# Kernel tuning notes

Hardware: AMD Instinct MI355X
Metric: run time of the kernel (lower is better)

Reference implementation:

```python
import jax, jax.numpy as jnp
import numpy as np

N = [100000, 50000, 25000, 12500]   # node frontier per hop (src of layer l = N[l], dst = N[l+1])
E = [800000, 400000, 200000]        # edges per sampled bipartite subgraph
IN, HID = 256, 256
N_LAYERS = 3


def setup_inputs() -> dict:
    key = jax.random.key(0)
    ks = jax.random.split(key, 20)
    inp = {"x": jax.random.normal(ks[0], (N[0], IN), dtype=jnp.float32)}
    for l in range(N_LAYERS):
        src = jax.random.randint(ks[1 + 2 * l], (E[l],), 0, N[l])
        dst = jax.random.randint(ks[2 + 2 * l], (E[l],), 0, N[l + 1])
        inp[f"edge_index_{l}"] = jnp.stack([src, dst]).astype(jnp.int64)
    for l in range(N_LAYERS):
        din = IN if l == 0 else HID
        s = din ** -0.5
        inp[f"W_l_{l}"] = jax.random.normal(ks[7 + 3 * l], (din, HID), jnp.float32) * s
        inp[f"b_l_{l}"] = jnp.zeros((HID,), jnp.float32)
        inp[f"W_r_{l}"] = jax.random.normal(ks[8 + 3 * l], (din, HID), jnp.float32) * s
    return inp


def _sage_layer(h, edge_index, num_dst, W_l, b_l, W_r):
    # PyG SAGEConv with mean aggregation:
    #   out = lin_l(mean_{j in N(i)} h_j) + lin_r(h_i),  h_i = h[:num_dst]
    src, dst = edge_index[0], edge_index[1]
    msg = h[src]                                                    # [E, d] gather
    summed = jax.ops.segment_sum(msg, dst, num_segments=num_dst)    # [num_dst, d]
    cnt = jax.ops.segment_sum(jnp.ones_like(dst, jnp.float32), dst, num_segments=num_dst)
    mean = summed / jnp.maximum(cnt, 1.0)[:, None]
    return mean @ W_l + b_l + h[:num_dst] @ W_r


def reference(x, edge_index_0, edge_index_1, edge_index_2,
              W_l_0, b_l_0, W_r_0, W_l_1, b_l_1, W_r_1, W_l_2, b_l_2, W_r_2):
    edges = [edge_index_0, edge_index_1, edge_index_2]
    params = [(W_l_0, b_l_0, W_r_0), (W_l_1, b_l_1, W_r_1), (W_l_2, b_l_2, W_r_2)]
    h = x
    for l in range(N_LAYERS):
        Wl, bl, Wr = params[l]
        h = _sage_layer(h, edges[l], N[l + 1], Wl, bl, Wr)
        if l != N_LAYERS - 1:
            h = jax.nn.relu(h)
    return h
```

## Files before the change

kernel.cpp:

```cpp
#include <hip/hip_runtime.h>
#include <hip/hip_bf16.h>

typedef __attribute__((ext_vector_type(8))) short bf16x8;
typedef __attribute__((ext_vector_type(4))) float f32x4;

__device__ inline unsigned short f2bf(float f) {
    union { float f; unsigned u; } v; v.f = f;
    unsigned r = v.u + 0x7fff + ((v.u >> 16) & 1);
    return (unsigned short)(r >> 16);
}
__device__ inline float bf2f(unsigned short u) {
    union { unsigned u; float f; } v; v.u = (unsigned)u << 16;
    return v.f;
}

#define SEG0_OFF 0
#define SEG1_OFF 50176
#define SEG2_OFF 75264
#define SEG_TOT  87808
#define NB0 196
#define NB1 98
#define NB2 49
#define NB_TOT 343
#define E_TOT 1400000

__constant__ const int c_segoff[3] = {SEG0_OFF, SEG1_OFF, SEG2_OFF};
__constant__ const int c_segM[3]   = {50000, 25000, 12500};
__constant__ const int c_Es[3]     = {800000, 400000, 200000};
__constant__ const int c_eoff[3]   = {0, 800000, 1200000};

__global__ void cvt_kernel(const float* __restrict__ x, unsigned short* __restrict__ xb, int n4) {
    int i = blockIdx.x * blockDim.x + threadIdx.x;
    if (i >= n4) return;
    float4 v = ((const float4*)x)[i];
    ushort4 o = { f2bf(v.x), f2bf(v.y), f2bf(v.z), f2bf(v.w) };
    ((ushort4*)xb)[i] = o;
}


__global__ void hist_all_kernel(const int* __restrict__ e0, const int* __restrict__ e1,
                                const int* __restrict__ e2, int* __restrict__ cnt) {
    int e = blockIdx.x * blockDim.x + threadIdx.x;
    if (e >= E_TOT) return;
    int l, el; const int* ex;
    if (e < 800000)       { l = 0; el = e;           ex = e0; }
    else if (e < 1200000) { l = 1; el = e - 800000;  ex = e1; }
    else                  { l = 2; el = e - 1200000; ex = e2; }
    int d = ex[c_Es[l] + el];
    atomicAdd(&cnt[c_segoff[l] + d], 1);
}

__device__ inline void seg_of_block(int b, int& seg, int& lb) {
    if (b < NB0)            { seg = 0; lb = b; }
    else if (b < NB0 + NB1) { seg = 1; lb = b - NB0; }
    else                    { seg = 2; lb = b - NB0 - NB1; }
}

__global__ void partial_kernel(const int* __restrict__ cnt, int* __restrict__ bsum) {
    int seg, lb; seg_of_block(blockIdx.x, seg, lb);
    __shared__ int sh[256];
    int t = threadIdx.x;
    sh[t] = cnt[c_segoff[seg] + lb * 256 + t];
    __syncthreads();
    #pragma unroll
    for (int off = 128; off > 0; off >>= 1) {
        if (t < off) sh[t] += sh[t + off];
        __syncthreads();
    }
    if (t == 0) bsum[seg * 256 + lb] = sh[0];
}

__global__ void scanb_kernel(int* __restrict__ bsum, int* __restrict__ rowptr) {
    const int nb[3] = {NB0, NB1, NB2};
    int s = blockIdx.x, t = threadIdx.x;
    __shared__ int sh[256];
    int v = (t < nb[s]) ? bsum[s * 256 + t] : 0;
    sh[t] = v;
    __syncthreads();
    #pragma unroll
    for (int off = 1; off < 256; off <<= 1) {
        int u = (t >= off) ? sh[t - off] : 0;
        __syncthreads();
        sh[t] += u;
        __syncthreads();
    }
    if (t < nb[s]) bsum[s * 256 + t] = sh[t] - v;
    if (t == 0) rowptr[c_segoff[s] + c_segM[s]] = c_Es[s];
}

__global__ void emit_kernel(const int* __restrict__ cnt, const int* __restrict__ bsum,
                            int* __restrict__ rowptr, int* __restrict__ cursor) {
    int seg, lb; seg_of_block(blockIdx.x, seg, lb);
    __shared__ int sh[256];
    int t = threadIdx.x;
    int li = lb * 256 + t;
    int idx = c_segoff[seg] + li;
    int v = cnt[idx];
    sh[t] = v;
    __syncthreads();
    #pragma unroll
    for (int off = 1; off < 256; off <<= 1) {
        int u = (t >= off) ? sh[t - off] : 0;
        __syncthreads();
        sh[t] += u;
        __syncthreads();
    }
    int excl = sh[t] - v + bsum[seg * 256 + lb];
    if (li < c_segM[seg]) { rowptr[idx] = excl; cursor[idx] = excl; }
}

__global__ void fill_all_kernel(const int* __restrict__ e0, const int* __restrict__ e1,
                                const int* __restrict__ e2,
                                int* __restrict__ cursor, int* __restrict__ eids) {
    int e = blockIdx.x * blockDim.x + threadIdx.x;
    if (e >= E_TOT) return;
    int l, el; const int* ex;
    if (e < 800000)       { l = 0; el = e;           ex = e0; }
    else if (e < 1200000) { l = 1; el = e - 800000;  ex = e1; }
    else                  { l = 2; el = e - 1200000; ex = e2; }
    int d = ex[c_Es[l] + el];
    int pos = atomicAdd(&cursor[c_segoff[l] + d], 1);
    eids[c_eoff[l] + pos] = ex[el];
}

__global__ void agg_pack_kernel(const unsigned short* __restrict__ hb,
                                const int* __restrict__ rowptr,
                                const int* __restrict__ eids,
                                int M, int Mpad,
                                unsigned short* __restrict__ X) {
    int lane = threadIdx.x & 63;
    int row = blockIdx.x * (blockDim.x >> 6) + (threadIdx.x >> 6);
    if (row >= Mpad) return;
    ushort4* Xv = (ushort4*)X;
    const ushort4* hv = (const ushort4*)hb;
    if (row >= M) {
        ushort4 z = {0, 0, 0, 0};
        Xv[(size_t)row * 128 + lane] = z;
        Xv[(size_t)row * 128 + 64 + lane] = z;
        return;
    }
    int beg = rowptr[row], end = rowptr[row + 1];
    float a0 = 0, a1 = 0, a2 = 0, a3 = 0;
    float b0 = 0, b1 = 0, b2 = 0, b3 = 0;
    int j = beg;
    for (; j + 4 <= end; j += 4) {
        int i0 = eids[j], i1 = eids[j + 1], i2 = eids[j + 2], i3 = eids[j + 3];
        ushort4 v0 = hv[(size_t)i0 * 64 + lane];
        ushort4 v1 = hv[(size_t)i1 * 64 + lane];
        ushort4 v2 = hv[(size_t)i2 * 64 + lane];
        ushort4 v3 = hv[(size_t)i3 * 64 + lane];
        a0 += bf2f(v0.x) + bf2f(v2.x); a1 += bf2f(v0.y) + bf2f(v2.y);
        a2 += bf2f(v0.z) + bf2f(v2.z); a3 += bf2f(v0.w) + bf2f(v2.w);
        b0 += bf2f(v1.x) + bf2f(v3.x); b1 += bf2f(v1.y) + bf2f(v3.y);
        b2 += bf2f(v1.z) + bf2f(v3.z); b3 += bf2f(v1.w) + bf2f(v3.w);
    }
    for (; j < end; ++j) {
        ushort4 v = hv[(size_t)eids[j] * 64 + lane];
        a0 += bf2f(v.x); a1 += bf2f(v.y); a2 += bf2f(v.z); a3 += bf2f(v.w);
    }
    float inv = 1.0f / fmaxf((float)(end - beg), 1.0f);
    ushort4 m;
    m.x = f2bf((a0 + b0) * inv); m.y = f2bf((a1 + b1) * inv);
    m.z = f2bf((a2 + b2) * inv); m.w = f2bf((a3 + b3) * inv);
    Xv[(size_t)row * 128 + lane] = m;
    Xv[(size_t)row * 128 + 64 + lane] = hv[(size_t)row * 64 + lane];
}

__global__ void convw_kernel(const float* __restrict__ Wl0, const float* __restrict__ Wr0,
                             const float* __restrict__ Wl1, const float* __restrict__ Wr1,
                             const float* __restrict__ Wl2, const float* __restrict__ Wr2,
                             unsigned short* __restrict__ Wsw) {
    int gid = blockIdx.x * blockDim.x + threadIdx.x;
    int l = gid >> 17;
    int r = gid & 131071;
    int k = r >> 8, c = r & 255;
    const float* W;
    if (k < 256) W = (l == 0) ? Wl0 : (l == 1) ? Wl1 : Wl2;
    else         W = (l == 0) ? Wr0 : (l == 1) ? Wr1 : Wr2;
    float v = W[(size_t)(k & 255) * 256 + c];
    Wsw[(size_t)l * 131072 + (size_t)(k >> 3) * 2048 + c * 8 + (k & 7)] = f2bf(v);
}

__global__ void gemm_kernel(const unsigned short* __restrict__ X,
                            const unsigned short* __restrict__ Wsw,
                            const float* __restrict__ bias,
                            float* __restrict__ outf, unsigned short* __restrict__ outb,
                            int M, int relu) {
    int tid = threadIdx.x;
    int wid = tid >> 6, lane = tid & 63;
    int lr = lane & 15, lg = lane >> 4;
    int r0 = blockIdx.x * 64;
    int c0 = wid * 64;
    f32x4 acc[4][4] = {};
    #pragma unroll 2
    for (int k0 = 0; k0 < 512; k0 += 32) {
        bf16x8 a[4];
        #pragma unroll
        for (int mf = 0; mf < 4; ++mf)
            a[mf] = *(const bf16x8*)(X + (size_t)(r0 + mf * 16 + lr) * 512 + k0 + lg * 8);
        #pragma unroll
        for (int nf = 0; nf < 4; ++nf) {
            bf16x8 b = *(const bf16x8*)(Wsw + ((size_t)(k0 >> 3) + lg) * 2048 +
                                        (size_t)(c0 + nf * 16 + lr) * 8);
            #pragma unroll
            for (int mf = 0; mf < 4; ++mf)
                acc[mf][nf] = __builtin_amdgcn_mfma_f32_16x16x32_bf16(a[mf], b, acc[mf][nf], 0, 0, 0);
        }
    }
    #pragma unroll
    for (int nf = 0; nf < 4; ++nf) {
        int col = c0 + nf * 16 + lr;
        float bv = bias[col];
        #pragma unroll
        for (int mf = 0; mf < 4; ++mf) {
            #pragma unroll
            for (int j = 0; j < 4; ++j) {
                int row = r0 + mf * 16 + lg * 4 + j;
                if (row < M) {
                    float v = acc[mf][nf][j] + bv;
                    if (relu) v = fmaxf(v, 0.0f);
                    size_t idx = (size_t)row * 256 + col;
                    if (outf) outf[idx] = v;
                    else      outb[idx] = f2bf(v);
                }
            }
        }
    }
}

extern "C" void kernel_launch(void* const* d_in, const int* in_sizes, int n_in,
                              void* d_out, int out_size, void* d_ws, size_t ws_size,
                              hipStream_t stream) {
    const float* x  = (const float*)d_in[0];
    const int*   e0 = (const int*)d_in[1];
    const int*   e1 = (const int*)d_in[2];
    const int*   e2 = (const int*)d_in[3];
    const float* Wl[3] = {(const float*)d_in[4], (const float*)d_in[7], (const float*)d_in[10]};
    const float* bl[3] = {(const float*)d_in[5], (const float*)d_in[8], (const float*)d_in[11]};
    const float* Wr[3] = {(const float*)d_in[6], (const float*)d_in[9], (const float*)d_in[12]};
    float* out = (float*)d_out;

    char* ws = (char*)d_ws;
    unsigned short* X      = (unsigned short*)(ws + 0);
    unsigned short* xb     = (unsigned short*)(ws + 51249152);
    unsigned short* h1b    = (unsigned short*)(ws + 102449152);
    unsigned short* h2b    = (unsigned short*)(ws + 128049152);
    unsigned short* Wsw    = (unsigned short*)(ws + 140849152);
    int*            cnt    = (int*)(ws + 141635584);
    int*            rowptr = (int*)(ws + 141986816);
    int*            cursor = (int*)(ws + 142338048);
    int*            bsum   = (int*)(ws + 142689280);
    int*            eids   = (int*)(ws + 142693376);

    const int Ns[4] = {100000, 50000, 25000, 12500};
    const int segoff[3] = {SEG0_OFF, SEG1_OFF, SEG2_OFF};
    const int eoff[3] = {0, 800000, 1200000};
    const unsigned short* hsrc[3] = {xb, h1b, h2b};

    hipMemsetAsync(cnt, 0, (size_t)SEG_TOT * 4, stream);
    cvt_kernel<<<(6400000 + 255) / 256, 256, 0, stream>>>(x, xb, 6400000);
    convw_kernel<<<1536, 256, 0, stream>>>(Wl[0], Wr[0], Wl[1], Wr[1], Wl[2], Wr[2], Wsw);

    hist_all_kernel<<<(E_TOT + 255) / 256, 256, 0, stream>>>(e0, e1, e2, cnt);
    partial_kernel<<<NB_TOT, 256, 0, stream>>>(cnt, bsum);
    scanb_kernel<<<3, 256, 0, stream>>>(bsum, rowptr);
    emit_kernel<<<NB_TOT, 256, 0, stream>>>(cnt, bsum, rowptr, cursor);
    fill_all_kernel<<<(E_TOT + 255) / 256, 256, 0, stream>>>(e0, e1, e2, cursor, eids);

    for (int l = 0; l < 3; ++l) {
        int Md = Ns[l + 1];
        int Mpad = (Md + 63) & ~63;
        agg_pack_kernel<<<Mpad / 4, 256, 0, stream>>>(
            hsrc[l], rowptr + segoff[l], eids + eoff[l], Md, Mpad, X);
        float* of = (l == 2) ? out : nullptr;
        unsigned short* ob = (l == 0) ? h1b : (l == 1) ? h2b : nullptr;
        gemm_kernel<<<Mpad / 64, 256, 0, stream>>>(
            X, Wsw + (size_t)l * 131072, bl[l], of, ob, Md, (l < 2) ? 1 : 0);
    }
}
```

Baseline: 586.7 us.

## Fuse prep kernels and record per-edge rank to drop fill atomics

```diff
diff --git a/kernel.cpp b/kernel.cpp
--- a/kernel.cpp
+++ b/kernel.cpp
@@ -23,31 +23,50 @@
 #define NB2 49
 #define NB_TOT 343
 #define E_TOT 1400000
+#define CVT_NB 25000
+#define CONVW_NB 1536
+#define HIST_NB 5469
 
 __constant__ const int c_segoff[3] = {SEG0_OFF, SEG1_OFF, SEG2_OFF};
 __constant__ const int c_segM[3]   = {50000, 25000, 12500};
 __constant__ const int c_Es[3]     = {800000, 400000, 200000};
 __constant__ const int c_eoff[3]   = {0, 800000, 1200000};
 
-__global__ void cvt_kernel(const float* __restrict__ x, unsigned short* __restrict__ xb, int n4) {
-    int i = blockIdx.x * blockDim.x + threadIdx.x;
-    if (i >= n4) return;
-    float4 v = ((const float4*)x)[i];
-    ushort4 o = { f2bf(v.x), f2bf(v.y), f2bf(v.z), f2bf(v.w) };
-    ((ushort4*)xb)[i] = o;
-}
-
-
-__global__ void hist_all_kernel(const int* __restrict__ e0, const int* __restrict__ e1,
-                                const int* __restrict__ e2, int* __restrict__ cnt) {
-    int e = blockIdx.x * blockDim.x + threadIdx.x;
-    if (e >= E_TOT) return;
-    int l, el; const int* ex;
-    if (e < 800000)       { l = 0; el = e;           ex = e0; }
-    else if (e < 1200000) { l = 1; el = e - 800000;  ex = e1; }
-    else                  { l = 2; el = e - 1200000; ex = e2; }
-    int d = ex[c_Es[l] + el];
-    atomicAdd(&cnt[c_segoff[l] + d], 1);
+__global__ void prep_kernel(const float* __restrict__ x, unsigned short* __restrict__ xb,
+                            const float* __restrict__ Wl0, const float* __restrict__ Wr0,
+                            const float* __restrict__ Wl1, const float* __restrict__ Wr1,
+                            const float* __restrict__ Wl2, const float* __restrict__ Wr2,
+                            unsigned short* __restrict__ Wsw,
+                            const int* __restrict__ e0, const int* __restrict__ e1,
+                            const int* __restrict__ e2,
+                            int* __restrict__ cnt, unsigned short* __restrict__ rank) {
+    int b = blockIdx.x, t = threadIdx.x;
+    if (b < CVT_NB) {
+        int i = b * 256 + t;
+        float4 v = ((const float4*)x)[i];
+        ushort4 o = { f2bf(v.x), f2bf(v.y), f2bf(v.z), f2bf(v.w) };
+        ((ushort4*)xb)[i] = o;
+    } else if (b < CVT_NB + CONVW_NB) {
+        int gid = (b - CVT_NB) * 256 + t;
+        int l = gid >> 17;
+        int r = gid & 131071;
+        int k = r >> 8, c = r & 255;
+        const float* W;
+        if (k < 256) W = (l == 0) ? Wl0 : (l == 1) ? Wl1 : Wl2;
+        else         W = (l == 0) ? Wr0 : (l == 1) ? Wr1 : Wr2;
+        float v = W[(size_t)(k & 255) * 256 + c];
+        Wsw[(size_t)l * 131072 + (size_t)(k >> 3) * 2048 + c * 8 + (k & 7)] = f2bf(v);
+    } else {
+        int e = (b - CVT_NB - CONVW_NB) * 256 + t;
+        if (e >= E_TOT) return;
+        int l, el; const int* ex;
+        if (e < 800000)       { l = 0; el = e;           ex = e0; }
+        else if (e < 1200000) { l = 1; el = e - 800000;  ex = e1; }
+        else                  { l = 2; el = e - 1200000; ex = e2; }
+        int d = ex[c_Es[l] + el];
+        int r = atomicAdd(&cnt[c_segoff[l] + d], 1);
+        rank[e] = (unsigned short)r;
+    }
 }
 
 __device__ inline void seg_of_block(int b, int& seg, int& lb) {
@@ -89,7 +108,7 @@
 }
 
 __global__ void emit_kernel(const int* __restrict__ cnt, const int* __restrict__ bsum,
-                            int* __restrict__ rowptr, int* __restrict__ cursor) {
+                            int* __restrict__ rowptr) {
     int seg, lb; seg_of_block(blockIdx.x, seg, lb);
     __shared__ int sh[256];
     int t = threadIdx.x;
@@ -106,12 +125,14 @@
         __syncthreads();
     }
     int excl = sh[t] - v + bsum[seg * 256 + lb];
-    if (li < c_segM[seg]) { rowptr[idx] = excl; cursor[idx] = excl; }
+    if (li < c_segM[seg]) rowptr[idx] = excl;
 }
 
 __global__ void fill_all_kernel(const int* __restrict__ e0, const int* __restrict__ e1,
                                 const int* __restrict__ e2,
-                                int* __restrict__ cursor, int* __restrict__ eids) {
+                                const int* __restrict__ rowptr,
+                                const unsigned short* __restrict__ rank,
+                                int* __restrict__ eids) {
     int e = blockIdx.x * blockDim.x + threadIdx.x;
     if (e >= E_TOT) return;
     int l, el; const int* ex;
@@ -119,7 +140,7 @@
     else if (e < 1200000) { l = 1; el = e - 800000;  ex = e1; }
     else                  { l = 2; el = e - 1200000; ex = e2; }
     int d = ex[c_Es[l] + el];
-    int pos = atomicAdd(&cursor[c_segoff[l] + d], 1);
+    int pos = rowptr[c_segoff[l] + d] + (int)rank[e];
     eids[c_eoff[l] + pos] = ex[el];
 }
 
@@ -164,21 +185,6 @@
     m.z = f2bf((a2 + b2) * inv); m.w = f2bf((a3 + b3) * inv);
     Xv[(size_t)row * 128 + lane] = m;
     Xv[(size_t)row * 128 + 64 + lane] = hv[(size_t)row * 64 + lane];
-}
-
-__global__ void convw_kernel(const float* __restrict__ Wl0, const float* __restrict__ Wr0,
-                             const float* __restrict__ Wl1, const float* __restrict__ Wr1,
-                             const float* __restrict__ Wl2, const float* __restrict__ Wr2,
-                             unsigned short* __restrict__ Wsw) {
-    int gid = blockIdx.x * blockDim.x + threadIdx.x;
-    int l = gid >> 17;
-    int r = gid & 131071;
-    int k = r >> 8, c = r & 255;
-    const float* W;
-    if (k < 256) W = (l == 0) ? Wl0 : (l == 1) ? Wl1 : Wl2;
-    else         W = (l == 0) ? Wr0 : (l == 1) ? Wr1 : Wr2;
-    float v = W[(size_t)(k & 255) * 256 + c];
-    Wsw[(size_t)l * 131072 + (size_t)(k >> 3) * 2048 + c * 8 + (k & 7)] = f2bf(v);
 }
 
 __global__ void gemm_kernel(const unsigned short* __restrict__ X,
@@ -242,15 +248,15 @@
 
     char* ws = (char*)d_ws;
     unsigned short* X      = (unsigned short*)(ws + 0);
+    unsigned short* rank   = (unsigned short*)(ws + 45000000);
     unsigned short* xb     = (unsigned short*)(ws + 51249152);
     unsigned short* h1b    = (unsigned short*)(ws + 102449152);
     unsigned short* h2b    = (unsigned short*)(ws + 128049152);
     unsigned short* Wsw    = (unsigned short*)(ws + 140849152);
     int*            cnt    = (int*)(ws + 141635584);
     int*            rowptr = (int*)(ws + 141986816);
-    int*            cursor = (int*)(ws + 142338048);
-    int*            bsum   = (int*)(ws + 142689280);
-    int*            eids   = (int*)(ws + 142693376);
+    int*            bsum   = (int*)(ws + 142338048);
+    int*            eids   = (int*)(ws + 142342144);
 
     const int Ns[4] = {100000, 50000, 25000, 12500};
     const int segoff[3] = {SEG0_OFF, SEG1_OFF, SEG2_OFF};
@@ -258,14 +264,12 @@
     const unsigned short* hsrc[3] = {xb, h1b, h2b};
 
     hipMemsetAsync(cnt, 0, (size_t)SEG_TOT * 4, stream);
-    cvt_kernel<<<(6400000 + 255) / 256, 256, 0, stream>>>(x, xb, 6400000);
-    convw_kernel<<<1536, 256, 0, stream>>>(Wl[0], Wr[0], Wl[1], Wr[1], Wl[2], Wr[2], Wsw);
-
-    hist_all_kernel<<<(E_TOT + 255) / 256, 256, 0, stream>>>(e0, e1, e2, cnt);
+    prep_kernel<<<CVT_NB + CONVW_NB + HIST_NB, 256, 0, stream>>>(
+        x, xb, Wl[0], Wr[0], Wl[1], Wr[1], Wl[2], Wr[2], Wsw, e0, e1, e2, cnt, rank);
     partial_kernel<<<NB_TOT, 256, 0, stream>>>(cnt, bsum);
     scanb_kernel<<<3, 256, 0, stream>>>(bsum, rowptr);
-    emit_kernel<<<NB_TOT, 256, 0, stream>>>(cnt, bsum, rowptr, cursor);
-    fill_all_kernel<<<(E_TOT + 255) / 256, 256, 0, stream>>>(e0, e1, e2, cursor, eids);
+    emit_kernel<<<NB_TOT, 256, 0, stream>>>(cnt, bsum, rowptr);
+    fill_all_kernel<<<(E_TOT + 255) / 256, 256, 0, stream>>>(e0, e1, e2, rowptr, rank, eids);
 
     for (int l = 0; l < 3; ++l) {
         int Md = Ns[l + 1];
```

New measurement: 499.6 us. 14.8% less time.
